# Kernel optimization log

Measured on AMD Instinct MI355X. Metric: run time of the kernel, lower is better.

The kernel has to match this reference:

```python
import jax, jax.numpy as jnp
import numpy as np
import math

B, S, D = 4, 2048, 1024      # batch, seq, d_model
E, F_EXP = 16, 512           # n_experts_ffn, d_expert_ffn
N_SHARED, K_FFN = 2, 4       # shared experts, routed top-k
N_ROUTED = E - N_SHARED


def setup_inputs() -> dict:
    key = jax.random.key(0)
    k0, k1, k2, k3, k4 = jax.random.split(key, 5)
    token_stream = jax.random.normal(k0, (B, S, D), jnp.float32)
    selection_input = jax.random.normal(k1, (B, S, D), jnp.float32)
    # init per reset_parameters (std_scale = 1.0)
    keys_w = jax.random.normal(k2, (E, D, F_EXP), jnp.float32) / math.sqrt(D)
    values_w = jax.random.normal(k3, (E, F_EXP, D), jnp.float32) / math.sqrt(E * F_EXP)
    expert_sel = jax.random.normal(k4, (E, D), jnp.float32) / math.sqrt(D)
    bias_ffn = jnp.zeros((E,), jnp.float32)  # load-balancing bias buffer
    return {
        "token_stream": token_stream,
        "selection_input": selection_input,
        "keys_w": keys_w,
        "values_w": values_w,
        "expert_sel": expert_sel,
        "bias_ffn": bias_ffn,
    }


def reference(token_stream, selection_input, keys_w, values_w, expert_sel, bias_ffn):
    # ---- routing: sigmoid affinity over all experts ----
    affinity = jax.nn.sigmoid(jnp.einsum("bsd,ed->bse", selection_input, expert_sel))  # [B,S,E]
    # top-k over routed experts (bias only affects ranking, not gathered affinity)
    _, routed_idx = jax.lax.top_k(affinity[..., :N_ROUTED] + bias_ffn[:N_ROUTED], K_FFN)  # [B,S,k]
    shared_idx = jnp.broadcast_to(
        jnp.arange(N_ROUTED, E, dtype=routed_idx.dtype), routed_idx.shape[:-1] + (N_SHARED,)
    )
    sel = jnp.concatenate([routed_idx, shared_idx], axis=-1)  # [B,S,K], K = k + shared
    aff_sel = jnp.take_along_axis(affinity, sel, axis=-1)     # [B,S,K]

    # ---- expert FFN (cvmm = gather / grouped GEMM / weighted scatter) ----
    # dense per-expert key projection, then gather selected experts
    scores_all = jnp.einsum("bsd,edf->bsef", token_stream, keys_w)        # [B,S,E,f]
    scores = jnp.take_along_axis(scores_all, sel[..., None], axis=2)      # [B,S,K,f]
    scores = jax.nn.silu(scores)

    # combine: out = sum_k aff_k * (scores_k @ values[sel_k])
    onehot = jax.nn.one_hot(sel, E, dtype=scores.dtype)                   # [B,S,K,E]
    dispatch = jnp.einsum("bskf,bske->bsef", scores * aff_sel[..., None], onehot)  # [B,S,E,f]
    out = jnp.einsum("bsef,efd->bsd", dispatch, values_w)                 # [B,S,D]
    return out, sel
```

## Files before the change

kernel.cpp:

```cpp
#include <hip/hip_runtime.h>

typedef short short8 __attribute__((ext_vector_type(8)));
typedef float f32x4 __attribute__((ext_vector_type(4)));
typedef unsigned short u16;

#define TOK_N 8192
#define DMODEL 1024
#define NEXP 16
#define FEXP 512
#define NROUTED 14
#define KSEL 6
#define MAXTILES 400

__device__ __forceinline__ u16 f2bf(float f) {
  unsigned u = __float_as_uint(f);
  u += 0x7fff + ((u >> 16) & 1);
  return (u16)(u >> 16);
}

typedef const __attribute__((address_space(1))) unsigned int* gas_p;
typedef __attribute__((address_space(3))) unsigned int* las_p;
__device__ __forceinline__ void gload_lds16(const void* g, void* l) {
  __builtin_amdgcn_global_load_lds((gas_p)g, (las_p)l, 16, 0, 0);
}

__global__ void cast_bf16_k(const float* __restrict__ in, u16* __restrict__ out, int n8) {
  int i = blockIdx.x * blockDim.x + threadIdx.x;
  if (i >= n8) return;
  const float4* p = (const float4*)(in + (size_t)i * 8);
  float4 a = p[0], b = p[1];
  short8 v;
  v[0] = (short)f2bf(a.x); v[1] = (short)f2bf(a.y); v[2] = (short)f2bf(a.z); v[3] = (short)f2bf(a.w);
  v[4] = (short)f2bf(b.x); v[5] = (short)f2bf(b.y); v[6] = (short)f2bf(b.z); v[7] = (short)f2bf(b.w);
  *(short8*)(out + (size_t)i * 8) = v;
}

__global__ void transpose_cast_k(const float* __restrict__ in, u16* __restrict__ out, int R, int C) {
  __shared__ u16 tile[32][33];
  int e = blockIdx.z;
  int c0 = blockIdx.x * 32, r0 = blockIdx.y * 32;
  int x = threadIdx.x, y = threadIdx.y;
  const float* ip = in + ((size_t)e * R + r0) * C + c0;
  #pragma unroll
  for (int i = 0; i < 4; i++)
    tile[y + 8 * i][x] = f2bf(ip[(size_t)(y + 8 * i) * C + x]);
  __syncthreads();
  u16* op = out + ((size_t)e * C + c0) * R + r0;
  #pragma unroll
  for (int i = 0; i < 4; i++)
    op[(size_t)(y + 8 * i) * R + x] = tile[x][y + 8 * i];
}

__global__ void routing_k(const float* __restrict__ selin, const float* __restrict__ esel,
                          const float* __restrict__ bias, float* __restrict__ out_sel,
                          unsigned* __restrict__ sel_pack, float* __restrict__ aff6) {
  int tok = blockIdx.x;
  int t = threadIdx.x;
  int e = t & 15, chunk = t >> 4;
  const float4* r4 = (const float4*)(selin + (size_t)tok * DMODEL + chunk * 64);
  const float4* w4 = (const float4*)(esel + (size_t)e * DMODEL + chunk * 64);
  float p = 0.f;
  #pragma unroll
  for (int i = 0; i < 16; i++) {
    float4 a = r4[i], b = w4[i];
    p += a.x * b.x + a.y * b.y + a.z * b.z + a.w * b.w;
  }
  __shared__ float part[16][17];
  __shared__ float aff[16];
  __shared__ float lbias[NROUTED];
  if (t < NROUTED) lbias[t] = bias[t];
  part[chunk][e] = p;
  __syncthreads();
  if (t < 16) {
    float s = 0.f;
    #pragma unroll
    for (int c = 0; c < 16; c++) s += part[c][t];
    aff[t] = 1.f / (1.f + expf(-s));
  }
  __syncthreads();
  if (t == 0) {
    unsigned pack = 0;
    unsigned taken = 0;
    #pragma unroll
    for (int k = 0; k < 4; k++) {
      float best = -3.4e38f; int bi = 0;
      for (int q = 0; q < NROUTED; q++) {
        if (taken & (1u << q)) continue;
        float v = aff[q] + lbias[q];
        if (v > best) { best = v; bi = q; }
      }
      taken |= 1u << bi;
      pack |= (unsigned)bi << (4 * k);
      out_sel[(size_t)tok * KSEL + k] = (float)bi;
      aff6[(size_t)tok * KSEL + k] = aff[bi];
    }
    pack |= 14u << 16; pack |= 15u << 20;
    out_sel[(size_t)tok * KSEL + 4] = 14.f;
    out_sel[(size_t)tok * KSEL + 5] = 15.f;
    aff6[(size_t)tok * KSEL + 4] = aff[14];
    aff6[(size_t)tok * KSEL + 5] = aff[15];
    sel_pack[tok] = pack;
  }
}

__global__ void scatter_k(const unsigned* __restrict__ sel_pack, const float* __restrict__ aff6,
                          int* __restrict__ counts, int* __restrict__ tokk,
                          float* __restrict__ affl) {
  __shared__ int lcnt[16], lbase[16], lcur[16];
  int t = threadIdx.x;
  int tok = blockIdx.x * 256 + t;
  if (t < 16) lcnt[t] = 0;
  __syncthreads();
  unsigned pack = sel_pack[tok];
  int eid[KSEL];
  #pragma unroll
  for (int k = 0; k < KSEL; k++) {
    eid[k] = (pack >> (4 * k)) & 15;
    atomicAdd(&lcnt[eid[k]], 1);
  }
  __syncthreads();
  if (t < 16) {
    lbase[t] = atomicAdd(&counts[t * 16], lcnt[t]);
    lcur[t] = 0;
  }
  __syncthreads();
  #pragma unroll
  for (int k = 0; k < KSEL; k++) {
    int e = eid[k];
    int slot = lbase[e] + atomicAdd(&lcur[e], 1);
    tokk[e * TOK_N + slot] = tok * 8 + k;
    affl[e * TOK_N + slot] = aff6[(size_t)tok * KSEL + k];
  }
}

__global__ void tilelist_k(const int* __restrict__ counts, int* __restrict__ tiles,
                           int* __restrict__ ntiles) {
  __shared__ int tc[16], pb[16];
  int t = threadIdx.x;
  if (t < 16) tc[t] = (counts[t * 16] + 127) >> 7;
  __syncthreads();
  if (t == 0) {
    int s = 0;
    for (int e = 0; e < 16; e++) { pb[e] = s; s += tc[e]; }
    *ntiles = s;
  }
  __syncthreads();
  if (t < 16) {
    int b = pb[t], n = tc[t];
    for (int i = 0; i < n; i++) tiles[b + i] = t | (i << 8);
  }
}

template<int AK, int PASS>
__global__ __launch_bounds__(256, 4) void moe_gemm_k(
    const u16* __restrict__ Abase, const u16* __restrict__ Bbase,
    const int* __restrict__ counts, const int* __restrict__ tokk,
    const float* __restrict__ affl, const int* __restrict__ tiles,
    const int* __restrict__ ntiles, u16* __restrict__ scores_out,
    float* __restrict__ out) {
  int slot = blockIdx.y;
  if (slot >= *ntiles) return;
  int desc = tiles[slot];
  int e = desc & 15;
  int m0 = (desc >> 8) << 7;
  int cnt = counts[e * 16];
  int n0 = blockIdx.x * 128;
  int t = threadIdx.x;
  int lane = t & 63, w = t >> 6;
  int wr = w >> 1, wc = w & 1;

  __shared__ u16 Al[2][128][64];
  __shared__ u16 Bl[2][128][64];

  const int* tl = tokk + e * TOK_N + m0;
  const float* al = affl + e * TOK_N + m0;
  const u16* Bp = Bbase + (size_t)e * 524288;

  f32x4 acc[4][4];
  #pragma unroll
  for (int m = 0; m < 4; m++)
    #pragma unroll
    for (int n = 0; n < 4; n++)
      acc[m][n] = (f32x4){0.f, 0.f, 0.f, 0.f};

  int jj = lane & 7, rl = lane >> 3;
  const u16* ag[4]; const u16* bg[4];
  #pragma unroll
  for (int r = 0; r < 4; r++) {
    int row = r * 32 + w * 8 + rl;
    int lr = (m0 + row < cnt) ? row : 0;
    int tk = tl[lr];
    int ar = (PASS == 2) ? (tk >> 3) : ((tk >> 3) * 6 + (tk & 7));
    int cs = (jj ^ (row & 7)) * 8;
    ag[r] = Abase + (size_t)ar * AK + cs;
    bg[r] = Bp + (size_t)(n0 + row) * AK + cs;
  }

#define STAGE(B, K0)                                             \
  _Pragma("unroll")                                              \
  for (int r = 0; r < 4; r++) {                                  \
    gload_lds16(ag[r] + (K0), &Al[B][r * 32 + w * 8][0]);        \
    gload_lds16(bg[r] + (K0), &Bl[B][r * 32 + w * 8][0]);        \
  }

#define COMPUTE(B)                                                         \
  _Pragma("unroll")                                                        \
  for (int kk = 0; kk < 2; kk++) {                                         \
    int lc = kk * 4 + (lane >> 4);                                         \
    short8 af[4], bf[4];                                                   \
    _Pragma("unroll")                                                      \
    for (int m = 0; m < 4; m++) {                                          \
      int row = wr * 64 + m * 16 + (lane & 15);                            \
      af[m] = *(const short8*)&Al[B][row][(lc ^ (row & 7)) * 8];           \
    }                                                                      \
    _Pragma("unroll")                                                      \
    for (int n = 0; n < 4; n++) {                                          \
      int row = wc * 64 + n * 16 + (lane & 15);                            \
      bf[n] = *(const short8*)&Bl[B][row][(lc ^ (row & 7)) * 8];           \
    }                                                                      \
    _Pragma("unroll")                                                      \
    for (int m = 0; m < 4; m++)                                            \
      _Pragma("unroll")                                                    \
      for (int n = 0; n < 4; n++)                                          \
        acc[m][n] = __builtin_amdgcn_mfma_f32_16x16x32_bf16(af[m], bf[n],  \
                                                            acc[m][n], 0, 0, 0); \
  }

  constexpr int NIT = AK / 64;
  STAGE(0, 0)
  __syncthreads();
  #pragma unroll 1
  for (int it = 0; it < NIT; it += 2) {
    if (it + 1 < NIT) STAGE(1, (it + 1) * 64)
    COMPUTE(0)
    __syncthreads();
    if (it + 2 < NIT) STAGE(0, (it + 2) * 64)
    COMPUTE(1)
    __syncthreads();
  }
#undef STAGE
#undef COMPUTE

  int cbase = n0 + wc * 64 + (lane & 15);
  #pragma unroll
  for (int m = 0; m < 4; m++) {
    int rbase = wr * 64 + m * 16 + ((lane >> 4) << 2);
    #pragma unroll
    for (int q = 0; q < 4; q++) {
      int row = rbase + q;
      if (m0 + row >= cnt) continue;
      int tk = tl[row];
      if (PASS == 2) {
        float aff = al[row];
        size_t base = (size_t)((tk >> 3) * 6 + (tk & 7)) * FEXP;
        #pragma unroll
        for (int n = 0; n < 4; n++) {
          float v = acc[m][n][q];
          float s = aff * v / (1.f + expf(-v));
          scores_out[base + cbase + n * 16] = f2bf(s);
        }
      } else {
        size_t base = (size_t)(tk >> 3) * DMODEL;
        #pragma unroll
        for (int n = 0; n < 4; n++)
          atomicAdd(&out[base + cbase + n * 16], acc[m][n][q]);
      }
    }
  }
}

extern "C" void kernel_launch(void* const* d_in, const int* in_sizes, int n_in,
                              void* d_out, int out_size, void* d_ws, size_t ws_size,
                              hipStream_t stream) {
  (void)in_sizes; (void)n_in; (void)out_size; (void)ws_size;
  const float* token_stream    = (const float*)d_in[0];
  const float* selection_input = (const float*)d_in[1];
  const float* keys_w          = (const float*)d_in[2];
  const float* values_w        = (const float*)d_in[3];
  const float* expert_sel      = (const float*)d_in[4];
  const float* bias_ffn        = (const float*)d_in[5];

  float* out     = (float*)d_out;
  float* out_sel = out + (size_t)TOK_N * DMODEL;

  char* ws = (char*)d_ws;
  u16*      Xbf      = (u16*)(ws + 0);
  u16*      keysT    = (u16*)(ws + 16777216);
  u16*      valuesT  = (u16*)(ws + 33554432);
  u16*      scoresbf = (u16*)(ws + 50331648);
  int*      counts   = (int*)(ws + 100663296);
  int*      tokk     = (int*)(ws + 100664320);
  float*    affl     = (float*)(ws + 101188608);
  unsigned* sel_pack = (unsigned*)(ws + 101712896);
  float*    aff6     = (float*)(ws + 101745664);
  int*      tiles    = (int*)(ws + 101942272);
  int*      ntiles   = (int*)(ws + 101946368);

  hipMemsetAsync(out, 0, (size_t)TOK_N * DMODEL * sizeof(float), stream);
  hipMemsetAsync(counts, 0, 1024, stream);

  cast_bf16_k<<<4096, 256, 0, stream>>>(token_stream, Xbf, TOK_N * DMODEL / 8);
  transpose_cast_k<<<dim3(16, 32, 16), dim3(32, 8), 0, stream>>>(keys_w, keysT, 1024, 512);
  transpose_cast_k<<<dim3(32, 16, 16), dim3(32, 8), 0, stream>>>(values_w, valuesT, 512, 1024);

  routing_k<<<TOK_N, 256, 0, stream>>>(selection_input, expert_sel, bias_ffn,
                                       out_sel, sel_pack, aff6);
  scatter_k<<<TOK_N / 256, 256, 0, stream>>>(sel_pack, aff6, counts, tokk, affl);
  tilelist_k<<<1, 64, 0, stream>>>(counts, tiles, ntiles);

  moe_gemm_k<1024, 2><<<dim3(4, MAXTILES), 256, 0, stream>>>(Xbf, keysT, counts, tokk, affl,
                                                             tiles, ntiles, scoresbf, nullptr);
  moe_gemm_k<512, 3><<<dim3(8, MAXTILES), 256, 0, stream>>>(scoresbf, valuesT, counts, tokk, affl,
                                                            tiles, ntiles, nullptr, out);
}
```

Measured before the change: 456.0 us.

## Load A operand fragments directly from global, drop A LDS staging

The grouped GEMM kernel stops staging the gathered A rows in shared memory. Each wave now owns 32 rows and all 128 columns, and reads its A fragments straight from global memory into registers, while only B goes through double-buffered LDS. This halves LDS footprint and global-to-LDS traffic per stage and removes A bank-conflict handling. In exchange A loads are issued synchronously inside the compute loop with no prefetch, so global latency may stall the MFMAs, and each B row in LDS is now read by all four waves.

```diff
diff --git a/kernel.cpp b/kernel.cpp
--- a/kernel.cpp
+++ b/kernel.cpp
@@ -167,61 +167,61 @@
   int n0 = blockIdx.x * 128;
   int t = threadIdx.x;
   int lane = t & 63, w = t >> 6;
-  int wr = w >> 1, wc = w & 1;
-
-  __shared__ u16 Al[2][128][64];
+
   __shared__ u16 Bl[2][128][64];
 
   const int* tl = tokk + e * TOK_N + m0;
   const float* al = affl + e * TOK_N + m0;
   const u16* Bp = Bbase + (size_t)e * 524288;
 
-  f32x4 acc[4][4];
-  #pragma unroll
-  for (int m = 0; m < 4; m++)
+  f32x4 acc[2][8];
+  #pragma unroll
+  for (int m = 0; m < 2; m++)
     #pragma unroll
-    for (int n = 0; n < 4; n++)
+    for (int n = 0; n < 8; n++)
       acc[m][n] = (f32x4){0.f, 0.f, 0.f, 0.f};
 
-  int jj = lane & 7, rl = lane >> 3;
-  const u16* ag[4]; const u16* bg[4];
-  #pragma unroll
-  for (int r = 0; r < 4; r++) {
-    int row = r * 32 + w * 8 + rl;
-    int lr = (m0 + row < cnt) ? row : 0;
+  const u16* arow[2];
+  #pragma unroll
+  for (int m = 0; m < 2; m++) {
+    int r = w * 32 + m * 16 + (lane & 15);
+    int lr = (m0 + r < cnt) ? r : 0;
     int tk = tl[lr];
     int ar = (PASS == 2) ? (tk >> 3) : ((tk >> 3) * 6 + (tk & 7));
-    int cs = (jj ^ (row & 7)) * 8;
-    ag[r] = Abase + (size_t)ar * AK + cs;
+    arow[m] = Abase + (size_t)ar * AK;
+  }
+  int acol = (lane >> 4) * 8;
+
+  const u16* bg[4];
+  #pragma unroll
+  for (int r = 0; r < 4; r++) {
+    int row = w * 32 + r * 8 + (lane >> 3);
+    int cs = ((lane & 7) ^ (lane >> 3)) * 8;
     bg[r] = Bp + (size_t)(n0 + row) * AK + cs;
   }
 
 #define STAGE(B, K0)                                             \
   _Pragma("unroll")                                              \
-  for (int r = 0; r < 4; r++) {                                  \
-    gload_lds16(ag[r] + (K0), &Al[B][r * 32 + w * 8][0]);        \
-    gload_lds16(bg[r] + (K0), &Bl[B][r * 32 + w * 8][0]);        \
-  }
-
-#define COMPUTE(B)                                                         \
+  for (int r = 0; r < 4; r++)                                    \
+    gload_lds16(bg[r] + (K0), &Bl[B][w * 32 + r * 8][0]);
+
+#define COMPUTE(B, K0)                                                     \
   _Pragma("unroll")                                                        \
   for (int kk = 0; kk < 2; kk++) {                                         \
+    short8 af[2], bf[8];                                                   \
+    _Pragma("unroll")                                                      \
+    for (int m = 0; m < 2; m++)                                            \
+      af[m] = *(const short8*)(arow[m] + (K0) + kk * 32 + acol);           \
     int lc = kk * 4 + (lane >> 4);                                         \
-    short8 af[4], bf[4];                                                   \
     _Pragma("unroll")                                                      \
-    for (int m = 0; m < 4; m++) {                                          \
-      int row = wr * 64 + m * 16 + (lane & 15);                            \
-      af[m] = *(const short8*)&Al[B][row][(lc ^ (row & 7)) * 8];           \
+    for (int n = 0; n < 8; n++) {                                          \
+      int row = n * 16 + (lane & 15);                                      \
+      bf[n] = *(const short8*)&Bl[B][row][(lc ^ (lane & 7)) * 8];          \
     }                                                                      \
     _Pragma("unroll")                                                      \
-    for (int n = 0; n < 4; n++) {                                          \
-      int row = wc * 64 + n * 16 + (lane & 15);                            \
-      bf[n] = *(const short8*)&Bl[B][row][(lc ^ (row & 7)) * 8];           \
-    }                                                                      \
-    _Pragma("unroll")                                                      \
-    for (int m = 0; m < 4; m++)                                            \
+    for (int m = 0; m < 2; m++)                                            \
       _Pragma("unroll")                                                    \
-      for (int n = 0; n < 4; n++)                                          \
+      for (int n = 0; n < 8; n++)                                          \
         acc[m][n] = __builtin_amdgcn_mfma_f32_16x16x32_bf16(af[m], bf[n],  \
                                                             acc[m][n], 0, 0, 0); \
   }
@@ -232,19 +232,19 @@
   #pragma unroll 1
   for (int it = 0; it < NIT; it += 2) {
     if (it + 1 < NIT) STAGE(1, (it + 1) * 64)
-    COMPUTE(0)
+    COMPUTE(0, it * 64)
     __syncthreads();
     if (it + 2 < NIT) STAGE(0, (it + 2) * 64)
-    COMPUTE(1)
+    COMPUTE(1, (it + 1) * 64)
     __syncthreads();
   }
 #undef STAGE
 #undef COMPUTE
 
-  int cbase = n0 + wc * 64 + (lane & 15);
-  #pragma unroll
-  for (int m = 0; m < 4; m++) {
-    int rbase = wr * 64 + m * 16 + ((lane >> 4) << 2);
+  int c0 = n0 + (lane & 15);
+  #pragma unroll
+  for (int m = 0; m < 2; m++) {
+    int rbase = w * 32 + m * 16 + ((lane >> 4) << 2);
     #pragma unroll
     for (int q = 0; q < 4; q++) {
       int row = rbase + q;
@@ -254,16 +254,16 @@
         float aff = al[row];
         size_t base = (size_t)((tk >> 3) * 6 + (tk & 7)) * FEXP;
         #pragma unroll
-        for (int n = 0; n < 4; n++) {
+        for (int n = 0; n < 8; n++) {
           float v = acc[m][n][q];
           float s = aff * v / (1.f + expf(-v));
-          scores_out[base + cbase + n * 16] = f2bf(s);
+          scores_out[base + c0 + n * 16] = f2bf(s);
         }
       } else {
         size_t base = (size_t)(tk >> 3) * DMODEL;
         #pragma unroll
-        for (int n = 0; n < 4; n++)
-          atomicAdd(&out[base + cbase + n * 16], acc[m][n][q]);
+        for (int n = 0; n < 8; n++)
+          atomicAdd(&out[base + c0 + n * 16], acc[m][n][q]);
       }
     }
   }
```

Result: slower. 509.7 us (+11.8%).
